# Kernel tuning notes

Hardware: AMD Instinct MI355X
Metric: run time of the kernel (lower is better)

The kernel has to match this reference:

```python
import jax, jax.numpy as jnp
import numpy as np

FEAT_DIM = 128
CUTOFF = 5.0


def setup_inputs() -> dict:
    key = jax.random.key(0)
    ks = jax.random.split(key, 12)
    B, NA, NC, F = 2, 1500, 64, FEAT_DIM
    inp = {
        "assign": jax.random.randint(ks[0], (B, NA), 0, NC),
        "h": jax.random.normal(ks[1], (B, NA, F), dtype=jnp.float32),
        "H": jax.random.normal(ks[2], (B, NC, F), dtype=jnp.float32),
        "cg_xyz": jax.random.normal(ks[3], (B, NC, 3), dtype=jnp.float32) * 3.0,
        "xyz": jax.random.normal(ks[4], (B, NA, 3), dtype=jnp.float32) * 3.0,
        "cg_adj": jax.random.uniform(ks[5], (B, NC, NC), dtype=jnp.float32),
        # dist_filter: Dense(F -> 3F)
        "Wf": jax.random.normal(ks[6], (F, 3 * F), dtype=jnp.float32) / np.sqrt(F),
        "bf": jnp.zeros((3 * F,), dtype=jnp.float32),
        # inv_dense: Dense(F->F, swish) -> Dense(F->3F)
        "W1": jax.random.normal(ks[7], (F, F), dtype=jnp.float32) / np.sqrt(F),
        "b1": jnp.zeros((F,), dtype=jnp.float32),
        "W2": jax.random.normal(ks[8], (F, 3 * F), dtype=jnp.float32) / np.sqrt(F),
        "b2": jnp.zeros((3 * F,), dtype=jnp.float32),
    }
    return inp


def reference(assign, h, H, cg_xyz, xyz, cg_adj, Wf, bf, W1, b1, W2, b2):
    F = h.shape[-1]
    # pairwise displacement: [B, n_cg, n_atoms, 3]
    r_iI = xyz[:, None, :, :] - cg_xyz[:, :, None, :]
    d_iI = jnp.sqrt(jnp.sum(r_iI * r_iI, axis=-1))          # [B, nc, na]
    unit = r_iI / d_iI[..., None]                            # [B, nc, na, 3]
    offset = jnp.linspace(0.0, CUTOFF, F)                    # [F]
    # invariant branch on atom features: swish MLP -> 3F
    phi = jax.nn.silu(h @ W1 + b1) @ W2 + b2                 # [B, na, 3F]
    # Gaussian RBF expansion of distances
    expanded_dist = jnp.exp(-jnp.square(d_iI[..., None] - offset))  # [B, nc, na, F]
    w_s = expanded_dist @ Wf + bf                            # [B, nc, na, 3F]
    filter_w = (w_s * phi[:, None, :, :]).reshape(*w_s.shape[:-1], F, 3)
    split_1 = filter_w[..., 1]                               # [B, nc, na, F]
    split_2 = filter_w[..., 2]                               # [B, nc, na, F]
    # v_i is all-zeros in the original, so the split_0 * v_i term vanishes
    unit_add = split_2[..., None] * unit[..., None, :]       # [B, nc, na, F, 3]
    dV = unit_add.sum(axis=2)                                # [B, nc, F, 3]
    dH = split_1.sum(axis=2)                                 # [B, nc, F]
    return (H + dH, dV)  # V_I is zeros, so V_I + dV == dV
```

## Files before the change

### kernel.cpp

```cpp
#include <hip/hip_runtime.h>
#include <cmath>

#define FDIM 128
#define NPTS 64
#define TDLT 0.16f
#define INVTDLT 6.25f
#define CLAMPF 62.0f

typedef __attribute__((ext_vector_type(8))) __bf16 bf16x8;
typedef __attribute__((ext_vector_type(4))) float f32x4;

__device__ inline unsigned short f2bf(float x) {
  unsigned int u = __float_as_uint(x);
  return (unsigned short)((u + 0x7FFFu + ((u >> 16) & 1u)) >> 16);
}
__device__ inline float bfw_lo(unsigned int w) { return __uint_as_float(w << 16); }
__device__ inline float bfw_hi(unsigned int w) { return __uint_as_float(w & 0xFFFF0000u); }
__device__ inline float rdlane(float v, int j) {
  return __int_as_float(__builtin_amdgcn_readlane(__float_as_int(v), j));
}

__global__ __launch_bounds__(64) void pack_frag_kernel(
    const float* __restrict__ W1, const float* __restrict__ W2,
    unsigned short* __restrict__ W1f, unsigned short* __restrict__ W2f) {
  const int ft = blockIdx.x, kt = blockIdx.y, z = blockIdx.z;
  const int lane = threadIdx.x;
  const float* W;
  unsigned short* out;
  int col, stride;
  if (z == 0) {
    if (ft >= 8) return;
    W = W1; out = W1f; col = ft * 16 + (lane & 15); stride = 128;
  } else {
    W = W2; out = W2f;
    col = 3 * ((ft & 7) * 16 + (lane & 15)) + 1 + (ft >> 3);
    stride = 384;
  }
  unsigned short g[8];
#pragma unroll
  for (int j = 0; j < 8; ++j) {
    const int k = kt * 32 + ((lane >> 4) << 3) + j;
    g[j] = f2bf(W[(size_t)k * stride + col]);
  }
  uint4 u;
  u.x = g[0] | ((unsigned int)g[1] << 16);
  u.y = g[2] | ((unsigned int)g[3] << 16);
  u.z = g[4] | ((unsigned int)g[5] << 16);
  u.w = g[6] | ((unsigned int)g[7] << 16);
  *(uint4*)&out[((size_t)(ft * 4 + kt) * 64 + lane) * 8] = u;
}

__global__ __launch_bounds__(256) void build_table_kernel(
    const float* __restrict__ Wf, const float* __restrict__ bf,
    unsigned int* __restrict__ Tq) {
  __shared__ float g[128];
  __shared__ float part[2][128][2];
  const int pt = blockIdx.x;
  const int tid = threadIdx.x;
  const int f = tid & 127;
  const int kh = tid >> 7;
  if (tid < 128) {
    const float dpt = pt * TDLT;
    const float o = tid * (5.0f / 127.0f);
    const float dd = dpt - o;
    g[tid] = expf(-dd * dd);
  }
  __syncthreads();
  float s0 = 0.f, s1 = 0.f;
#pragma unroll 8
  for (int kk = 0; kk < 64; ++kk) {
    const int k = kh * 64 + kk;
    s0 = fmaf(g[k], Wf[(size_t)k * 384 + 3 * f + 1], s0);
    s1 = fmaf(g[k], Wf[(size_t)k * 384 + 3 * f + 2], s1);
  }
  part[kh][f][0] = s0;
  part[kh][f][1] = s1;
  __syncthreads();
  if (tid < 128) {
    const float v0 = part[0][tid][0] + part[1][tid][0] + bf[3 * tid + 1];
    const float v1 = part[0][tid][1] + part[1][tid][1] + bf[3 * tid + 2];
    const unsigned int word = f2bf(v0) | ((unsigned int)f2bf(v1) << 16);
    Tq[((size_t)pt * 64 + (tid & 63)) * 2 + (tid >> 6)] = word;
  }
}

__global__ __launch_bounds__(256) void phi_mfma_kernel(
    const float* __restrict__ h, const unsigned short* __restrict__ W1f,
    const float* __restrict__ b1, const unsigned short* __restrict__ W2f,
    const float* __restrict__ b2, unsigned int* __restrict__ phiQ, int BNA) {
  __shared__ __bf16 hA[4 * 64 * 8];
  __shared__ unsigned short tS[16 * 128];
  const int tid = threadIdx.x;
  const int lane = tid & 63;
  const int w = tid >> 6;
  const int hw = lane >> 4, lcol = lane & 15;
  const int r0 = blockIdx.x * 16;

  {
    const int gl = tid & 63;
    const int kt = tid >> 6;
    const int row = gl & 15;
    const int k0 = kt * 32 + ((gl >> 4) << 3);
    const int gr = r0 + row;
    bf16x8 v;
    if (gr < BNA) {
      const float4 f0 = *(const float4*)&h[(size_t)gr * FDIM + k0];
      const float4 f1 = *(const float4*)&h[(size_t)gr * FDIM + k0 + 4];
      v[0] = (__bf16)f0.x; v[1] = (__bf16)f0.y; v[2] = (__bf16)f0.z; v[3] = (__bf16)f0.w;
      v[4] = (__bf16)f1.x; v[5] = (__bf16)f1.y; v[6] = (__bf16)f1.z; v[7] = (__bf16)f1.w;
    } else {
#pragma unroll
      for (int j = 0; j < 8; ++j) v[j] = (__bf16)0.0f;
    }
    *reinterpret_cast<bf16x8*>(&hA[tid * 8]) = v;
  }

  bf16x8 B1[2][4];
#pragma unroll
  for (int ftl = 0; ftl < 2; ++ftl)
#pragma unroll
    for (int kt = 0; kt < 4; ++kt)
      B1[ftl][kt] = *reinterpret_cast<const bf16x8*>(
          &W1f[(((size_t)(w * 2 + ftl) * 4 + kt) * 64 + lane) * 8]);
  float b1v[2];
#pragma unroll
  for (int ftl = 0; ftl < 2; ++ftl) b1v[ftl] = b1[w * 32 + ftl * 16 + lcol];
  __syncthreads();

  {
    bf16x8 ga[4];
#pragma unroll
    for (int kt = 0; kt < 4; ++kt)
      ga[kt] = *reinterpret_cast<const bf16x8*>(&hA[(kt * 64 + lane) * 8]);
    f32x4 acc[2];
    acc[0] = (f32x4){0.f, 0.f, 0.f, 0.f};
    acc[1] = (f32x4){0.f, 0.f, 0.f, 0.f};
#pragma unroll
    for (int ftl = 0; ftl < 2; ++ftl)
#pragma unroll
      for (int kt = 0; kt < 4; ++kt)
        acc[ftl] = __builtin_amdgcn_mfma_f32_16x16x32_bf16(ga[kt], B1[ftl][kt], acc[ftl], 0, 0, 0);
#pragma unroll
    for (int ftl = 0; ftl < 2; ++ftl)
#pragma unroll
      for (int reg = 0; reg < 4; ++reg) {
        const int row = hw * 4 + reg;
        const int fcol = w * 32 + ftl * 16 + lcol;
        const float x = acc[ftl][reg] + b1v[ftl];
        const float t = x / (1.0f + __expf(-x));
        const int byte = (row * 256 + fcol * 2) ^ ((row & 7) << 4);
        *(unsigned short*)((char*)tS + byte) = f2bf(t);
      }
  }

  bf16x8 B2[2][2][4];
  float b2v[2][2];
#pragma unroll
  for (int ftl = 0; ftl < 2; ++ftl) {
    const int fcol = w * 32 + ftl * 16 + lcol;
#pragma unroll
    for (int s_ = 0; s_ < 2; ++s_) {
      const int ft = s_ * 8 + w * 2 + ftl;
#pragma unroll
      for (int kt = 0; kt < 4; ++kt)
        B2[ftl][s_][kt] = *reinterpret_cast<const bf16x8*>(
            &W2f[(((size_t)ft * 4 + kt) * 64 + lane) * 8]);
      b2v[ftl][s_] = b2[3 * fcol + 1 + s_];
    }
  }
  __syncthreads();

  {
    bf16x8 ta[4];
#pragma unroll
    for (int kt = 0; kt < 4; ++kt) {
      const int row = lcol;
      const int k0 = kt * 32 + hw * 8;
      const int byte = (row * 256 + k0 * 2) ^ ((row & 7) << 4);
      ta[kt] = *reinterpret_cast<const bf16x8*>((const char*)tS + byte);
    }
    f32x4 acc[2][2];
#pragma unroll
    for (int ftl = 0; ftl < 2; ++ftl)
#pragma unroll
      for (int s_ = 0; s_ < 2; ++s_) acc[ftl][s_] = (f32x4){0.f, 0.f, 0.f, 0.f};
#pragma unroll
    for (int ftl = 0; ftl < 2; ++ftl)
#pragma unroll
      for (int s_ = 0; s_ < 2; ++s_)
#pragma unroll
        for (int kt = 0; kt < 4; ++kt)
          acc[ftl][s_] = __builtin_amdgcn_mfma_f32_16x16x32_bf16(ta[kt], B2[ftl][s_][kt],
                                                                 acc[ftl][s_], 0, 0, 0);
#pragma unroll
    for (int ftl = 0; ftl < 2; ++ftl)
#pragma unroll
      for (int reg = 0; reg < 4; ++reg) {
        const int row = hw * 4 + reg;
        const int gr = r0 + row;
        if (gr < BNA) {
          const float v0 = acc[ftl][0][reg] + b2v[ftl][0];
          const float v1 = acc[ftl][1][reg] + b2v[ftl][1];
          const unsigned int word = f2bf(v0) | ((unsigned int)f2bf(v1) << 16);
          phiQ[(size_t)gr * FDIM + w * 32 + ftl * 16 + lcol] = word;
        }
      }
  }
}

template <int ASPLIT>
__global__ __launch_bounds__(256, 4) void enc_main_kernel(
    const float* __restrict__ xyz, const float* __restrict__ cg_xyz,
    const unsigned int* __restrict__ Tg, const unsigned int* __restrict__ phiQ,
    float* __restrict__ pH, float* __restrict__ pV,
    int NA, int NC, int BNC, int BNA) {
  __shared__ uint2 Tl[NPTS * 64];
  __shared__ float red[4][64][8];

  const int az = blockIdx.x;
  const int c = blockIdx.y;
  const int b = blockIdx.z;
  const int bc = b * NC + c;
  const int tid = threadIdx.x;
  const int l = tid & 63;
  const int wv = tid >> 6;
  const size_t arow = (size_t)b * NA;

  {
    const uint4* src4 = (const uint4*)Tg;
    uint4* dst4 = (uint4*)Tl;
#pragma unroll
    for (int i = 0; i < 8; ++i) dst4[tid + i * 256] = src4[tid + i * 256];
  }

  const float cgx = cg_xyz[bc * 3 + 0];
  const float cgy = cg_xyz[bc * 3 + 1];
  const float cgz = cg_xyz[bc * 3 + 2];

  const int APA = (NA + ASPLIT - 1) / ASPLIT;
  const int a0 = az * APA;
  const int a_end = min(NA, a0 + APA);
  const int cnt = (a_end > a0) ? (a_end - a0) : 0;
  const int wcnt = (cnt + 3) >> 2;
  const int aw0 = a0 + wv * wcnt;
  const int aw1 = min(a_end, aw0 + wcnt);

  __syncthreads();

  float accH0 = 0.f, accH1 = 0.f;
  float accV0[3] = {0.f, 0.f, 0.f};
  float accV1[3] = {0.f, 0.f, 0.f};

  for (int base = aw0; base < aw1; base += 64) {
    int n = aw1 - base;
    if (n > 64) n = 64;

    float fidx = 0.f, ux = 0.f, uy = 0.f, uz = 0.f;
    if (l < n) {
      const int a = base + l;
      const float dx = xyz[(arow + a) * 3 + 0] - cgx;
      const float dy = xyz[(arow + a) * 3 + 1] - cgy;
      const float dz = xyz[(arow + a) * 3 + 2] - cgz;
      const float d = sqrtf(dx * dx + dy * dy + dz * dz);
      const float inv = 1.0f / d;
      ux = dx * inv; uy = dy * inv; uz = dz * inv;
      fidx = fminf(d * INVTDLT, CLAMPF);
    }

    const unsigned int* pq = phiQ + ((size_t)(arow + base)) * FDIM + l;

    for (int jb = 0; jb < n; jb += 4) {
      uint2 t0[4], t1[4];
      float fr[4], sux[4], suy[4], suz[4];
      unsigned int pa[4], pb[4];
#pragma unroll
      for (int q = 0; q < 4; ++q) {
        const int jj = jb + q;
        const int jl = jj & 63;
        const float sf = rdlane(fidx, jl);
        const int idx = (int)sf;
        fr[q] = sf - (float)idx;
        t0[q] = Tl[idx * 64 + l];
        t1[q] = Tl[idx * 64 + 64 + l];
        sux[q] = rdlane(ux, jl);
        suy[q] = rdlane(uy, jl);
        suz[q] = rdlane(uz, jl);
        if (jj < n) {
          pa[q] = pq[(size_t)jj * FDIM];
          pb[q] = pq[(size_t)jj * FDIM + 64];
        } else {
          pa[q] = 0u; pb[q] = 0u;
        }
      }
#pragma unroll
      for (int q = 0; q < 4; ++q) {
        const float A1 = bfw_lo(t0[q].x), A2 = bfw_hi(t0[q].x);
        const float B1 = bfw_lo(t1[q].x), B2 = bfw_hi(t1[q].x);
        const float C1 = bfw_lo(t0[q].y), C2 = bfw_hi(t0[q].y);
        const float D1 = bfw_lo(t1[q].y), D2 = bfw_hi(t1[q].y);
        const float S1a = fmaf(fr[q], B1 - A1, A1);
        const float S2a = fmaf(fr[q], B2 - A2, A2);
        const float S1b = fmaf(fr[q], D1 - C1, C1);
        const float S2b = fmaf(fr[q], D2 - C2, C2);

        const float p1a = bfw_lo(pa[q]), p2a = bfw_hi(pa[q]);
        const float p1b = bfw_lo(pb[q]), p2b = bfw_hi(pb[q]);

        accH0 = fmaf(S1a, p1a, accH0);
        accH1 = fmaf(S1b, p1b, accH1);
        const float t2a = S2a * p2a;
        const float t2b = S2b * p2b;
        accV0[0] = fmaf(t2a, sux[q], accV0[0]);
        accV0[1] = fmaf(t2a, suy[q], accV0[1]);
        accV0[2] = fmaf(t2a, suz[q], accV0[2]);
        accV1[0] = fmaf(t2b, sux[q], accV1[0]);
        accV1[1] = fmaf(t2b, suy[q], accV1[1]);
        accV1[2] = fmaf(t2b, suz[q], accV1[2]);
      }
    }
  }

  red[wv][l][0] = accH0;  red[wv][l][1] = accH1;
  red[wv][l][2] = accV0[0]; red[wv][l][3] = accV0[1]; red[wv][l][4] = accV0[2];
  red[wv][l][5] = accV1[0]; red[wv][l][6] = accV1[1]; red[wv][l][7] = accV1[2];
  __syncthreads();
#pragma unroll
  for (int i = 0; i < 2; ++i) {
    const int slot = tid + i * 256;
    const int sl = slot >> 3;
    const int comp = slot & 7;
    const float v = red[0][sl][comp] + red[1][sl][comp] +
                    red[2][sl][comp] + red[3][sl][comp];
    if (comp == 0) {
      pH[((size_t)az * BNC + bc) * FDIM + sl] = v;
    } else if (comp == 1) {
      pH[((size_t)az * BNC + bc) * FDIM + sl + 64] = v;
    } else if (comp < 5) {
      pV[(((size_t)az * BNC + bc) * FDIM + sl) * 3 + (comp - 2)] = v;
    } else {
      pV[(((size_t)az * BNC + bc) * FDIM + sl + 64) * 3 + (comp - 5)] = v;
    }
  }
}

template <int P>
__global__ __launch_bounds__(FDIM) void reduce_kernel(
    const float* __restrict__ H, const float* __restrict__ pH, const float* __restrict__ pV,
    float* __restrict__ out, int BNC) {
  const int bc = blockIdx.x;
  const int f = threadIdx.x;
  float s = H[(size_t)bc * FDIM + f];
#pragma unroll
  for (int p = 0; p < P; ++p) s += pH[((size_t)p * BNC + bc) * FDIM + f];
  out[(size_t)bc * FDIM + f] = s;
  float* outV = out + (size_t)BNC * FDIM;
#pragma unroll
  for (int x = 0; x < 3; ++x) {
    float v = 0.f;
#pragma unroll
    for (int p = 0; p < P; ++p) v += pV[(((size_t)p * BNC + bc) * FDIM + f) * 3 + x];
    outV[((size_t)bc * FDIM + f) * 3 + x] = v;
  }
}

extern "C" void kernel_launch(void* const* d_in, const int* in_sizes, int n_in,
                              void* d_out, int out_size, void* d_ws, size_t ws_size,
                              hipStream_t stream) {
  const float* h      = (const float*)d_in[1];
  const float* Hc     = (const float*)d_in[2];
  const float* cg_xyz = (const float*)d_in[3];
  const float* xyz    = (const float*)d_in[4];
  const float* Wf     = (const float*)d_in[6];
  const float* bf     = (const float*)d_in[7];
  const float* W1     = (const float*)d_in[8];
  const float* b1     = (const float*)d_in[9];
  const float* W2     = (const float*)d_in[10];
  const float* b2     = (const float*)d_in[11];

  const int BNC = in_sizes[2] / FDIM;
  const int NC  = in_sizes[5] / BNC;
  const int B   = BNC / NC;
  const int NA  = in_sizes[0] / B;
  const int BNA = B * NA;
  constexpr int ASPLIT = 8;

  char* wsb = (char*)d_ws;
  unsigned short* W1f = (unsigned short*)wsb;
  unsigned short* W2f = (unsigned short*)(wsb + 32768);
  unsigned int*  Tq   = (unsigned int*)(wsb + 32768 + 65536);
  unsigned int*  phiQ = (unsigned int*)(wsb + 2 * 65536);
  char* pp = wsb + 2 * 65536 + (size_t)BNA * FDIM * 4;
  float* pH = (float*)pp;                  pp += (size_t)ASPLIT * BNC * FDIM * 4;
  float* pV = (float*)pp;

  pack_frag_kernel<<<dim3(16, 4, 2), 64, 0, stream>>>(W1, W2, W1f, W2f);
  build_table_kernel<<<NPTS, 256, 0, stream>>>(Wf, bf, Tq);
  phi_mfma_kernel<<<(BNA + 15) / 16, 256, 0, stream>>>(h, W1f, b1, W2f, b2, phiQ, BNA);
  enc_main_kernel<ASPLIT><<<dim3(ASPLIT, NC, B), 256, 0, stream>>>(
      xyz, cg_xyz, Tq, phiQ, pH, pV, NA, NC, BNC, BNA);
  reduce_kernel<ASPLIT><<<BNC, FDIM, 0, stream>>>(Hc, pH, pV, (float*)d_out, BNC);
}
```

Before: 36.84 us.

## Merge prep kernels and use 512-thread blocks with fewer atom splits

Fuses the weight-fragment packing and RBF table build into a single prep kernel, removing one launch. The main kernel moves to 512-thread blocks (8 waves) with ASPLIT halved, so each block copies the table once for twice as many atoms. The cross-wave reduction now reuses the table's shared memory, which frees the separate reduction buffer. Fewer blocks per batch-cluster pair also means fewer partials for the final reduce, at the cost of less grid-level parallelism.

After: 33.23 us. 9.8% less time.

```diff
diff --git a/kernel.cpp b/kernel.cpp
--- a/kernel.cpp
+++ b/kernel.cpp
@@ -20,67 +20,69 @@
   return __int_as_float(__builtin_amdgcn_readlane(__float_as_int(v), j));
 }
 
-__global__ __launch_bounds__(64) void pack_frag_kernel(
+__global__ __launch_bounds__(256) void prep_kernel(
     const float* __restrict__ W1, const float* __restrict__ W2,
-    unsigned short* __restrict__ W1f, unsigned short* __restrict__ W2f) {
-  const int ft = blockIdx.x, kt = blockIdx.y, z = blockIdx.z;
-  const int lane = threadIdx.x;
-  const float* W;
-  unsigned short* out;
-  int col, stride;
-  if (z == 0) {
-    if (ft >= 8) return;
-    W = W1; out = W1f; col = ft * 16 + (lane & 15); stride = 128;
+    const float* __restrict__ Wf, const float* __restrict__ bf,
+    unsigned short* __restrict__ W1f, unsigned short* __restrict__ W2f,
+    unsigned int* __restrict__ Tq) {
+  const int bid = blockIdx.x;
+  const int tid = threadIdx.x;
+  if (bid < 128) {
+    if (tid >= 64) return;
+    const int ft = bid & 15, kt = (bid >> 4) & 3, z = bid >> 6;
+    const int lane = tid;
+    const float* W;
+    unsigned short* out;
+    int col, stride;
+    if (z == 0) {
+      if (ft >= 8) return;
+      W = W1; out = W1f; col = ft * 16 + (lane & 15); stride = 128;
+    } else {
+      W = W2; out = W2f;
+      col = 3 * ((ft & 7) * 16 + (lane & 15)) + 1 + (ft >> 3);
+      stride = 384;
+    }
+    unsigned short g[8];
+#pragma unroll
+    for (int j = 0; j < 8; ++j) {
+      const int k = kt * 32 + ((lane >> 4) << 3) + j;
+      g[j] = f2bf(W[(size_t)k * stride + col]);
+    }
+    uint4 u;
+    u.x = g[0] | ((unsigned int)g[1] << 16);
+    u.y = g[2] | ((unsigned int)g[3] << 16);
+    u.z = g[4] | ((unsigned int)g[5] << 16);
+    u.w = g[6] | ((unsigned int)g[7] << 16);
+    *(uint4*)&out[((size_t)(ft * 4 + kt) * 64 + lane) * 8] = u;
   } else {
-    W = W2; out = W2f;
-    col = 3 * ((ft & 7) * 16 + (lane & 15)) + 1 + (ft >> 3);
-    stride = 384;
-  }
-  unsigned short g[8];
-#pragma unroll
-  for (int j = 0; j < 8; ++j) {
-    const int k = kt * 32 + ((lane >> 4) << 3) + j;
-    g[j] = f2bf(W[(size_t)k * stride + col]);
-  }
-  uint4 u;
-  u.x = g[0] | ((unsigned int)g[1] << 16);
-  u.y = g[2] | ((unsigned int)g[3] << 16);
-  u.z = g[4] | ((unsigned int)g[5] << 16);
-  u.w = g[6] | ((unsigned int)g[7] << 16);
-  *(uint4*)&out[((size_t)(ft * 4 + kt) * 64 + lane) * 8] = u;
-}
-
-__global__ __launch_bounds__(256) void build_table_kernel(
-    const float* __restrict__ Wf, const float* __restrict__ bf,
-    unsigned int* __restrict__ Tq) {
-  __shared__ float g[128];
-  __shared__ float part[2][128][2];
-  const int pt = blockIdx.x;
-  const int tid = threadIdx.x;
-  const int f = tid & 127;
-  const int kh = tid >> 7;
-  if (tid < 128) {
-    const float dpt = pt * TDLT;
-    const float o = tid * (5.0f / 127.0f);
-    const float dd = dpt - o;
-    g[tid] = expf(-dd * dd);
-  }
-  __syncthreads();
-  float s0 = 0.f, s1 = 0.f;
+    __shared__ float g[128];
+    __shared__ float part[2][128][2];
+    const int pt = bid - 128;
+    const int f = tid & 127;
+    const int kh = tid >> 7;
+    if (tid < 128) {
+      const float dpt = pt * TDLT;
+      const float o = tid * (5.0f / 127.0f);
+      const float dd = dpt - o;
+      g[tid] = expf(-dd * dd);
+    }
+    __syncthreads();
+    float s0 = 0.f, s1 = 0.f;
 #pragma unroll 8
-  for (int kk = 0; kk < 64; ++kk) {
-    const int k = kh * 64 + kk;
-    s0 = fmaf(g[k], Wf[(size_t)k * 384 + 3 * f + 1], s0);
-    s1 = fmaf(g[k], Wf[(size_t)k * 384 + 3 * f + 2], s1);
-  }
-  part[kh][f][0] = s0;
-  part[kh][f][1] = s1;
-  __syncthreads();
-  if (tid < 128) {
-    const float v0 = part[0][tid][0] + part[1][tid][0] + bf[3 * tid + 1];
-    const float v1 = part[0][tid][1] + part[1][tid][1] + bf[3 * tid + 2];
-    const unsigned int word = f2bf(v0) | ((unsigned int)f2bf(v1) << 16);
-    Tq[((size_t)pt * 64 + (tid & 63)) * 2 + (tid >> 6)] = word;
+    for (int kk = 0; kk < 64; ++kk) {
+      const int k = kh * 64 + kk;
+      s0 = fmaf(g[k], Wf[(size_t)k * 384 + 3 * f + 1], s0);
+      s1 = fmaf(g[k], Wf[(size_t)k * 384 + 3 * f + 2], s1);
+    }
+    part[kh][f][0] = s0;
+    part[kh][f][1] = s1;
+    __syncthreads();
+    if (tid < 128) {
+      const float v0 = part[0][tid][0] + part[1][tid][0] + bf[3 * tid + 1];
+      const float v1 = part[0][tid][1] + part[1][tid][1] + bf[3 * tid + 2];
+      const unsigned int word = f2bf(v0) | ((unsigned int)f2bf(v1) << 16);
+      Tq[((size_t)pt * 64 + (tid & 63)) * 2 + (tid >> 6)] = word;
+    }
   }
 }
 
@@ -209,13 +211,12 @@
 }
 
 template <int ASPLIT>
-__global__ __launch_bounds__(256, 4) void enc_main_kernel(
+__global__ __launch_bounds__(512, 6) void enc_main_kernel(
     const float* __restrict__ xyz, const float* __restrict__ cg_xyz,
     const unsigned int* __restrict__ Tg, const unsigned int* __restrict__ phiQ,
     float* __restrict__ pH, float* __restrict__ pV,
     int NA, int NC, int BNC, int BNA) {
   __shared__ uint2 Tl[NPTS * 64];
-  __shared__ float red[4][64][8];
 
   const int az = blockIdx.x;
   const int c = blockIdx.y;
@@ -230,7 +231,7 @@
     const uint4* src4 = (const uint4*)Tg;
     uint4* dst4 = (uint4*)Tl;
 #pragma unroll
-    for (int i = 0; i < 8; ++i) dst4[tid + i * 256] = src4[tid + i * 256];
+    for (int i = 0; i < 4; ++i) dst4[tid + i * 512] = src4[tid + i * 512];
   }
 
   const float cgx = cg_xyz[bc * 3 + 0];
@@ -241,7 +242,7 @@
   const int a0 = az * APA;
   const int a_end = min(NA, a0 + APA);
   const int cnt = (a_end > a0) ? (a_end - a0) : 0;
-  const int wcnt = (cnt + 3) >> 2;
+  const int wcnt = (cnt + 7) >> 3;
   const int aw0 = a0 + wv * wcnt;
   const int aw1 = min(a_end, aw0 + wcnt);
 
@@ -320,17 +321,23 @@
     }
   }
 
-  red[wv][l][0] = accH0;  red[wv][l][1] = accH1;
-  red[wv][l][2] = accV0[0]; red[wv][l][3] = accV0[1]; red[wv][l][4] = accV0[2];
-  red[wv][l][5] = accV1[0]; red[wv][l][6] = accV1[1]; red[wv][l][7] = accV1[2];
   __syncthreads();
-#pragma unroll
-  for (int i = 0; i < 2; ++i) {
-    const int slot = tid + i * 256;
-    const int sl = slot >> 3;
-    const int comp = slot & 7;
-    const float v = red[0][sl][comp] + red[1][sl][comp] +
-                    red[2][sl][comp] + red[3][sl][comp];
+  float* red = (float*)Tl;
+  red[0 * 512 + wv * 64 + l] = accH0;
+  red[1 * 512 + wv * 64 + l] = accH1;
+  red[2 * 512 + wv * 64 + l] = accV0[0];
+  red[3 * 512 + wv * 64 + l] = accV0[1];
+  red[4 * 512 + wv * 64 + l] = accV0[2];
+  red[5 * 512 + wv * 64 + l] = accV1[0];
+  red[6 * 512 + wv * 64 + l] = accV1[1];
+  red[7 * 512 + wv * 64 + l] = accV1[2];
+  __syncthreads();
+  {
+    const int comp = tid >> 6;
+    const int sl = tid & 63;
+    float v = 0.f;
+#pragma unroll
+    for (int w8 = 0; w8 < 8; ++w8) v += red[comp * 512 + w8 * 64 + sl];
     if (comp == 0) {
       pH[((size_t)az * BNC + bc) * FDIM + sl] = v;
     } else if (comp == 1) {
@@ -382,7 +389,7 @@
   const int B   = BNC / NC;
   const int NA  = in_sizes[0] / B;
   const int BNA = B * NA;
-  constexpr int ASPLIT = 8;
+  constexpr int ASPLIT = 4;
 
   char* wsb = (char*)d_ws;
   unsigned short* W1f = (unsigned short*)wsb;
@@ -393,10 +400,9 @@
   float* pH = (float*)pp;                  pp += (size_t)ASPLIT * BNC * FDIM * 4;
   float* pV = (float*)pp;
 
-  pack_frag_kernel<<<dim3(16, 4, 2), 64, 0, stream>>>(W1, W2, W1f, W2f);
-  build_table_kernel<<<NPTS, 256, 0, stream>>>(Wf, bf, Tq);
+  prep_kernel<<<128 + NPTS, 256, 0, stream>>>(W1, W2, Wf, bf, W1f, W2f, Tq);
   phi_mfma_kernel<<<(BNA + 15) / 16, 256, 0, stream>>>(h, W1f, b1, W2f, b2, phiQ, BNA);
-  enc_main_kernel<ASPLIT><<<dim3(ASPLIT, NC, B), 256, 0, stream>>>(
+  enc_main_kernel<ASPLIT><<<dim3(ASPLIT, NC, B), 512, 0, stream>>>(
       xyz, cg_xyz, Tq, phiQ, pH, pV, NA, NC, BNC, BNA);
   reduce_kernel<ASPLIT><<<BNC, FDIM, 0, stream>>>(Hc, pH, pV, (float*)d_out, BNC);
 }
```
